# Kernel tuning notes

Hardware: AMD Instinct MI355X
Metric: run time of the kernel (lower is better)

## Reference

```python
import jax, jax.numpy as jnp
import numpy as np

TABLE_SIZE = 256
N_EMBD = 768
B, T = 2, 1024
VOCAB = TABLE_SIZE * TABLE_SIZE


def setup_inputs() -> dict:
    key = jax.random.key(0)
    k1, k2, k3, k4 = jax.random.split(key, 4)
    hidden_states = jax.random.normal(k1, (B, T, N_EMBD), dtype=jnp.float32)
    target_ids = jax.random.randint(k2, (B, T), 0, VOCAB, dtype=jnp.int32).astype(jnp.int64)
    W_row = jax.random.normal(k3, (TABLE_SIZE, N_EMBD), dtype=jnp.float32) * 0.02
    b_row = jnp.zeros((TABLE_SIZE,), dtype=jnp.float32)
    col_weight = jax.random.normal(k4, (TABLE_SIZE, N_EMBD, TABLE_SIZE), dtype=jnp.float32) * 0.02
    col_bias = jnp.zeros((TABLE_SIZE, TABLE_SIZE), dtype=jnp.float32)
    return {
        "hidden_states": hidden_states,
        "target_ids": target_ids,
        "W_row": W_row,
        "b_row": b_row,
        "col_weight": col_weight,
        "col_bias": col_bias,
    }


def reference(hidden_states, target_ids, W_row, b_row, col_weight, col_bias):
    table_size = col_weight.shape[0]
    # row head: (B,T,R)
    row_logits = jnp.einsum("btd,rd->btr", hidden_states, W_row) + b_row
    # codebook.lookup: factor token id over table_size x table_size grid
    row_ids = (target_ids // table_size).reshape(-1)  # (N,)
    col_ids = (target_ids % table_size).reshape(-1)   # (N,)
    hs_flat = hidden_states.reshape(-1, hidden_states.shape[-1])  # (N,d)
    # per-token hard-routed column projection (the gather + baddbmm)
    W_tok = col_weight[row_ids]                       # (N,d,C)
    col_logits = jnp.einsum("nd,ndc->nc", hs_flat, W_tok) + col_bias[row_ids]
    # cross-entropy losses (mean over tokens)
    lp_row = jax.nn.log_softmax(row_logits.reshape(-1, table_size), axis=-1)
    loss_row = -jnp.take_along_axis(lp_row, row_ids[:, None], axis=1).mean()
    lp_col = jax.nn.log_softmax(col_logits, axis=-1)
    loss_col = -jnp.take_along_axis(lp_col, col_ids[:, None], axis=1).mean()
    return loss_row + loss_col
```

## Files before the change

### kernel.cpp

```cpp
#include <hip/hip_runtime.h>
#include <math.h>

#define TABLE 256
#define DIM   768
#define NCH   6
#define DCH   128
#define KTOK  12
#define CAP   64

__device__ __forceinline__ float4 f4zero() { return make_float4(0.f, 0.f, 0.f, 0.f); }

__global__ __launch_bounds__(256) void k_ztrans(
    const float* __restrict__ Wrow,
    float* __restrict__ WrowT,
    int* __restrict__ counts)
{
    const int d = blockIdx.x;
    const int c = threadIdx.x;
    if (d == 0) counts[c] = 0;
    WrowT[(size_t)d * TABLE + c] = Wrow[(size_t)c * DIM + d];
}

__global__ __launch_bounds__(256) void k_bucket(
    const int* __restrict__ tgt, int ntok,
    int* __restrict__ counts, int* __restrict__ bucket)
{
    const int n = blockIdx.x * 256 + threadIdx.x;
    if (n >= ntok) return;
    const int r = tgt[n] >> 8;
    const int pos = atomicAdd(&counts[r], 1);
    if (pos < CAP) bucket[r * CAP + pos] = n;
}

__device__ __forceinline__ void stream_pass(
    const float4* __restrict__ slab4,
    const float*  __restrict__ hs,
    const int* tk,
    int nvalid,
    int dbase,
    float* __restrict__ outp,
    int lane)
{
    int off[KTOK];
    #pragma unroll
    for (int j = 0; j < KTOK; ++j) off[j] = tk[j] * DIM + dbase;

    float4 acc[KTOK];
    #pragma unroll
    for (int j = 0; j < KTOK; ++j) acc[j] = f4zero();

    for (int dq = 0; dq < DCH / 4; ++dq) {
        float4 hv[KTOK];
        #pragma unroll
        for (int j = 0; j < KTOK; ++j)
            hv[j] = reinterpret_cast<const float4*>(hs + off[j])[dq];
        #pragma unroll
        for (int dd = 0; dd < 4; ++dd) {
            const float4 wv = slab4[(size_t)(dq * 4 + dd) * 64 + lane];
            #pragma unroll
            for (int j = 0; j < KTOK; ++j) {
                const float h = (dd == 0) ? hv[j].x : (dd == 1) ? hv[j].y
                              : (dd == 2) ? hv[j].z : hv[j].w;
                acc[j].x = fmaf(h, wv.x, acc[j].x);
                acc[j].y = fmaf(h, wv.y, acc[j].y);
                acc[j].z = fmaf(h, wv.z, acc[j].z);
                acc[j].w = fmaf(h, wv.w, acc[j].w);
            }
        }
    }

    #pragma unroll
    for (int j = 0; j < KTOK; ++j)
        if (j < nvalid)
            reinterpret_cast<float4*>(outp + (size_t)tk[j] * TABLE)[lane] = acc[j];
}

__global__ __launch_bounds__(64) void k_stream(
    const float* __restrict__ hs,
    const float* __restrict__ WrowT,
    const float* __restrict__ CW,
    const int* __restrict__ counts,
    const int* __restrict__ bucket,
    float* __restrict__ row_part,
    float* __restrict__ col_part,
    int ntok)
{
    const int bid  = blockIdx.x;
    const int lane = threadIdx.x;
    const int ncol = 256 * NCH;
    int tk[KTOK];

    if (bid < ncol) {
        const int r     = bid & 255;
        const int chunk = bid >> 8;
        const int cnt = min(counts[r], CAP);
        if (cnt == 0) return;
        const float4* slab4 = reinterpret_cast<const float4*>(
            CW + (size_t)r * DIM * TABLE + (size_t)chunk * DCH * TABLE);
        float* outp = col_part + (size_t)chunk * ntok * TABLE;
        for (int base = 0; base < cnt; base += KTOK) {
            #pragma unroll
            for (int j = 0; j < KTOK; ++j) {
                const int idx = (base + j < cnt) ? (base + j) : base;
                tk[j] = __builtin_amdgcn_readfirstlane(bucket[r * CAP + idx]);
            }
            stream_pass(slab4, hs, tk, min(KTOK, cnt - base),
                        chunk * DCH, outp, lane);
        }
    } else {
        const int b      = bid - ncol;
        const int ntiles = (ntok + KTOK - 1) / KTOK;
        const int tile   = b % ntiles;
        const int chunk  = b / ntiles;
        const int cnt    = min(KTOK, ntok - tile * KTOK);
        #pragma unroll
        for (int j = 0; j < KTOK; ++j) {
            const int idx = (j < cnt) ? j : 0;
            tk[j] = tile * KTOK + idx;
        }
        const float4* slab4 = reinterpret_cast<const float4*>(
            WrowT + (size_t)chunk * DCH * TABLE);
        float* outp = row_part + (size_t)chunk * ntok * TABLE;
        stream_pass(slab4, hs, tk, cnt, chunk * DCH, outp, lane);
    }
}

__device__ __forceinline__ float wave_nll(float4 v, int target, int lane) {
    float m = fmaxf(fmaxf(v.x, v.y), fmaxf(v.z, v.w));
    #pragma unroll
    for (int off = 32; off > 0; off >>= 1) m = fmaxf(m, __shfl_xor(m, off));
    float e = expf(v.x - m) + expf(v.y - m) + expf(v.z - m) + expf(v.w - m);
    float lt = 0.f;
    if (lane == (target >> 2)) {
        const int j = target & 3;
        lt = (j == 0) ? v.x : (j == 1) ? v.y : (j == 2) ? v.z : v.w;
    }
    #pragma unroll
    for (int off = 32; off > 0; off >>= 1) {
        e  += __shfl_xor(e, off);
        lt += __shfl_xor(lt, off);
    }
    return m + logf(e) - lt;
}

__global__ __launch_bounds__(256) void k_nll2(
    const float* __restrict__ row_part,
    const float* __restrict__ col_part,
    const float* __restrict__ brow,
    const float* __restrict__ cbias,
    const int* __restrict__ tgt, int ntok,
    float* __restrict__ per_tok)
{
    const int n = blockIdx.x * 4 + (threadIdx.x >> 6);
    if (n >= ntok) return;
    const int lane = threadIdx.x & 63;
    const int t = tgt[n];
    const int r = t >> 8;

    float4 rl = reinterpret_cast<const float4*>(brow)[lane];
    float4 cl = reinterpret_cast<const float4*>(cbias + (size_t)r * TABLE)[lane];
    #pragma unroll
    for (int ch = 0; ch < NCH; ++ch) {
        const float4 a = reinterpret_cast<const float4*>(
            row_part + ((size_t)ch * ntok + n) * TABLE)[lane];
        const float4 b = reinterpret_cast<const float4*>(
            col_part + ((size_t)ch * ntok + n) * TABLE)[lane];
        rl.x += a.x; rl.y += a.y; rl.z += a.z; rl.w += a.w;
        cl.x += b.x; cl.y += b.y; cl.z += b.z; cl.w += b.w;
    }
    const float lr = wave_nll(rl, r, lane);
    const float lc = wave_nll(cl, t & 255, lane);
    if (lane == 0) per_tok[n] = lr + lc;
}

__global__ __launch_bounds__(256) void k_reduce(
    const float* __restrict__ per_tok, int ntok, float* __restrict__ out)
{
    __shared__ float red[256];
    const int c = threadIdx.x;
    float s = 0.f;
    for (int i = c; i < ntok; i += 256) s += per_tok[i];
    red[c] = s;
    __syncthreads();
    #pragma unroll
    for (int k = 128; k > 0; k >>= 1) {
        if (c < k) red[c] += red[c + k];
        __syncthreads();
    }
    if (c == 0) out[0] = red[0] / (float)ntok;
}

extern "C" void kernel_launch(void* const* d_in, const int* in_sizes, int n_in,
                              void* d_out, int out_size, void* d_ws, size_t ws_size,
                              hipStream_t stream) {
    const float* hs    = (const float*)d_in[0];
    const int*   tgt   = (const int*)d_in[1];
    const float* Wrow  = (const float*)d_in[2];
    const float* brow  = (const float*)d_in[3];
    const float* CW    = (const float*)d_in[4];
    const float* cbias = (const float*)d_in[5];
    float* out = (float*)d_out;

    const int ntok = in_sizes[1];

    char* ws = (char*)d_ws;
    int*   counts   = (int*)(ws);
    int*   bucket   = (int*)(ws + 1024);
    float* WrowT    = (float*)(ws + 1024 + 256 * CAP * 4);
    char*  p0       = (char*)WrowT + (size_t)DIM * TABLE * 4;
    float* row_part = (float*)p0;
    float* col_part = row_part + (size_t)NCH * ntok * TABLE;
    float* per_tok  = col_part + (size_t)NCH * ntok * TABLE;

    const int ntiles = (ntok + KTOK - 1) / KTOK;
    const int nblk   = 256 * NCH + ntiles * NCH;

    k_ztrans <<<DIM, 256, 0, stream>>>(Wrow, WrowT, counts);
    k_bucket <<<(ntok + 255) / 256, 256, 0, stream>>>(tgt, ntok, counts, bucket);
    k_stream <<<nblk, 64, 0, stream>>>(hs, WrowT, CW, counts, bucket,
                                       row_part, col_part, ntok);
    k_nll2   <<<(ntok + 3) / 4, 256, 0, stream>>>(row_part, col_part, brow, cbias,
                                                  tgt, ntok, per_tok);
    k_reduce <<<1, 256, 0, stream>>>(per_tok, ntok, out);
}
```

Before: 82.07 us.

## Split column dimension across two waves per block-chunk in stream kernel

Each k_stream block now covers half of the 256 output columns (float2 per lane instead of float4), and twice as many blocks are launched. This halves per-thread accumulator registers and doubles parallelism, which should improve occupancy and latency hiding. The cost is that each block re-reads the hidden-state vectors for its tokens, so hs traffic doubles, and per-lane weight loads become narrower. An unroll-2 hint is also added to the d loop.

```diff
diff --git a/kernel.cpp b/kernel.cpp
--- a/kernel.cpp
+++ b/kernel.cpp
@@ -8,7 +8,7 @@
 #define KTOK  12
 #define CAP   64
 
-__device__ __forceinline__ float4 f4zero() { return make_float4(0.f, 0.f, 0.f, 0.f); }
+__device__ __forceinline__ float2 f2zero() { return make_float2(0.f, 0.f); }
 
 __global__ __launch_bounds__(256) void k_ztrans(
     const float* __restrict__ Wrow,
@@ -33,11 +33,12 @@
 }
 
 __device__ __forceinline__ void stream_pass(
-    const float4* __restrict__ slab4,
-    const float*  __restrict__ hs,
+    const float* __restrict__ slab,
+    const float* __restrict__ hs,
     const int* tk,
     int nvalid,
     int dbase,
+    int cbase,
     float* __restrict__ outp,
     int lane)
 {
@@ -45,10 +46,13 @@
     #pragma unroll
     for (int j = 0; j < KTOK; ++j) off[j] = tk[j] * DIM + dbase;
 
-    float4 acc[KTOK];
-    #pragma unroll
-    for (int j = 0; j < KTOK; ++j) acc[j] = f4zero();
-
+    float2 acc[KTOK];
+    #pragma unroll
+    for (int j = 0; j < KTOK; ++j) acc[j] = f2zero();
+
+    const float* sl = slab + cbase + 2 * lane;
+
+    #pragma unroll 2
     for (int dq = 0; dq < DCH / 4; ++dq) {
         float4 hv[KTOK];
         #pragma unroll
@@ -56,15 +60,14 @@
             hv[j] = reinterpret_cast<const float4*>(hs + off[j])[dq];
         #pragma unroll
         for (int dd = 0; dd < 4; ++dd) {
-            const float4 wv = slab4[(size_t)(dq * 4 + dd) * 64 + lane];
+            const float2 wv = *reinterpret_cast<const float2*>(
+                sl + (size_t)(dq * 4 + dd) * TABLE);
             #pragma unroll
             for (int j = 0; j < KTOK; ++j) {
                 const float h = (dd == 0) ? hv[j].x : (dd == 1) ? hv[j].y
                               : (dd == 2) ? hv[j].z : hv[j].w;
                 acc[j].x = fmaf(h, wv.x, acc[j].x);
                 acc[j].y = fmaf(h, wv.y, acc[j].y);
-                acc[j].z = fmaf(h, wv.z, acc[j].z);
-                acc[j].w = fmaf(h, wv.w, acc[j].w);
             }
         }
     }
@@ -72,7 +75,8 @@
     #pragma unroll
     for (int j = 0; j < KTOK; ++j)
         if (j < nvalid)
-            reinterpret_cast<float4*>(outp + (size_t)tk[j] * TABLE)[lane] = acc[j];
+            *reinterpret_cast<float2*>(outp + (size_t)tk[j] * TABLE + cbase + 2 * lane)
+                = acc[j];
 }
 
 __global__ __launch_bounds__(64) void k_stream(
@@ -87,16 +91,17 @@
 {
     const int bid  = blockIdx.x;
     const int lane = threadIdx.x;
-    const int ncol = 256 * NCH;
+    const int ncol = 256 * NCH * 2;
     int tk[KTOK];
 
     if (bid < ncol) {
         const int r     = bid & 255;
-        const int chunk = bid >> 8;
+        const int rest  = bid >> 8;
+        const int chunk = rest >> 1;
+        const int cbase = (rest & 1) * 128;
         const int cnt = min(counts[r], CAP);
         if (cnt == 0) return;
-        const float4* slab4 = reinterpret_cast<const float4*>(
-            CW + (size_t)r * DIM * TABLE + (size_t)chunk * DCH * TABLE);
+        const float* slab = CW + (size_t)r * DIM * TABLE + (size_t)chunk * DCH * TABLE;
         float* outp = col_part + (size_t)chunk * ntok * TABLE;
         for (int base = 0; base < cnt; base += KTOK) {
             #pragma unroll
@@ -104,24 +109,25 @@
                 const int idx = (base + j < cnt) ? (base + j) : base;
                 tk[j] = __builtin_amdgcn_readfirstlane(bucket[r * CAP + idx]);
             }
-            stream_pass(slab4, hs, tk, min(KTOK, cnt - base),
-                        chunk * DCH, outp, lane);
+            stream_pass(slab, hs, tk, min(KTOK, cnt - base),
+                        chunk * DCH, cbase, outp, lane);
         }
     } else {
         const int b      = bid - ncol;
         const int ntiles = (ntok + KTOK - 1) / KTOK;
         const int tile   = b % ntiles;
-        const int chunk  = b / ntiles;
+        const int rest   = b / ntiles;
+        const int chunk  = rest >> 1;
+        const int cbase  = (rest & 1) * 128;
         const int cnt    = min(KTOK, ntok - tile * KTOK);
         #pragma unroll
         for (int j = 0; j < KTOK; ++j) {
             const int idx = (j < cnt) ? j : 0;
             tk[j] = tile * KTOK + idx;
         }
-        const float4* slab4 = reinterpret_cast<const float4*>(
-            WrowT + (size_t)chunk * DCH * TABLE);
+        const float* slab = WrowT + (size_t)chunk * DCH * TABLE;
         float* outp = row_part + (size_t)chunk * ntok * TABLE;
-        stream_pass(slab4, hs, tk, cnt, chunk * DCH, outp, lane);
+        stream_pass(slab, hs, tk, cnt, chunk * DCH, cbase, outp, lane);
     }
 }
 
@@ -213,7 +219,7 @@
     float* per_tok  = col_part + (size_t)NCH * ntok * TABLE;
 
     const int ntiles = (ntok + KTOK - 1) / KTOK;
-    const int nblk   = 256 * NCH + ntiles * NCH;
+    const int nblk   = 256 * NCH * 2 + ntiles * NCH * 2;
 
     k_ztrans <<<DIM, 256, 0, stream>>>(Wrow, WrowT, counts);
     k_bucket <<<(ntok + 255) / 256, 256, 0, stream>>>(tgt, ntok, counts, bucket);
```

After: 76.27 us. -7.1%, faster.

## Stage weight slab through LDS with async global_load_lds ring buffer

Applied to the files above, without the earlier changes.

Hidden-state chunks for the token tile are staged into shared memory once per pass. Weight slab rows are prefetched into a 16-row LDS ring using global-to-LDS async loads, with manual vmcnt waits so loads overlap the FMA compute. The aim is to hide global memory latency in the per-row streaming kernel. It adds LDS usage, hand-tuned waitcnt sequencing that is fragile, and extra LDS read traffic.

```diff
diff --git a/kernel.cpp b/kernel.cpp
--- a/kernel.cpp
+++ b/kernel.cpp
@@ -7,8 +7,7 @@
 #define DCH   128
 #define KTOK  12
 #define CAP   64
-
-__device__ __forceinline__ float4 f4zero() { return make_float4(0.f, 0.f, 0.f, 0.f); }
+#define WIN   16
 
 __global__ __launch_bounds__(256) void k_ztrans(
     const float* __restrict__ Wrow,
@@ -32,42 +31,85 @@
     if (pos < CAP) bucket[r * CAP + pos] = n;
 }
 
+__device__ __forceinline__ void async_row(const float* g, float4* l, int lane) {
+    __builtin_amdgcn_global_load_lds(
+        (const __attribute__((address_space(1))) void*)(g + 4 * lane),
+        (__attribute__((address_space(3))) void*)l, 16, 0, 0);
+}
+
 __device__ __forceinline__ void stream_pass(
-    const float4* __restrict__ slab4,
-    const float*  __restrict__ hs,
+    const float* __restrict__ slab,
+    const float* __restrict__ hs,
     const int* tk,
     int nvalid,
     int dbase,
+    float4 (*slab_lds)[64],
+    float* hs_lds,
     float* __restrict__ outp,
     int lane)
 {
-    int off[KTOK];
-    #pragma unroll
-    for (int j = 0; j < KTOK; ++j) off[j] = tk[j] * DIM + dbase;
+    const int half = lane >> 5;
+    const int q    = lane & 31;
+    #pragma unroll
+    for (int i = 0; i < KTOK / 2; ++i) {
+        const int tt = (half == 0) ? tk[2 * i] : tk[2 * i + 1];
+        const float4 v = *reinterpret_cast<const float4*>(
+            hs + (size_t)tt * DIM + dbase + 4 * q);
+        *reinterpret_cast<float4*>(hs_lds + (2 * i + half) * DCH + 4 * q) = v;
+    }
+    asm volatile("s_waitcnt vmcnt(0) lgkmcnt(0)" ::: "memory");
+
+    #pragma unroll
+    for (int r = 0; r < WIN; ++r)
+        async_row(slab + (size_t)r * TABLE, &slab_lds[r][0], lane);
 
     float4 acc[KTOK];
     #pragma unroll
-    for (int j = 0; j < KTOK; ++j) acc[j] = f4zero();
-
-    for (int dq = 0; dq < DCH / 4; ++dq) {
+    for (int j = 0; j < KTOK; ++j) acc[j] = make_float4(0.f, 0.f, 0.f, 0.f);
+
+    auto compute_group = [&](int g) {
         float4 hv[KTOK];
         #pragma unroll
         for (int j = 0; j < KTOK; ++j)
-            hv[j] = reinterpret_cast<const float4*>(hs + off[j])[dq];
+            hv[j] = *reinterpret_cast<const float4*>(hs_lds + j * DCH + 4 * g);
         #pragma unroll
-        for (int dd = 0; dd < 4; ++dd) {
-            const float4 wv = slab4[(size_t)(dq * 4 + dd) * 64 + lane];
+        for (int k = 0; k < 4; ++k) {
+            const float4 wv = slab_lds[(4 * g + k) & (WIN - 1)][lane];
             #pragma unroll
             for (int j = 0; j < KTOK; ++j) {
-                const float h = (dd == 0) ? hv[j].x : (dd == 1) ? hv[j].y
-                              : (dd == 2) ? hv[j].z : hv[j].w;
+                const float h = (k == 0) ? hv[j].x : (k == 1) ? hv[j].y
+                              : (k == 2) ? hv[j].z : hv[j].w;
                 acc[j].x = fmaf(h, wv.x, acc[j].x);
                 acc[j].y = fmaf(h, wv.y, acc[j].y);
                 acc[j].z = fmaf(h, wv.z, acc[j].z);
                 acc[j].w = fmaf(h, wv.w, acc[j].w);
             }
         }
-    }
+    };
+
+    for (int g = 0; g < 29; ++g) {
+        asm volatile("s_waitcnt vmcnt(12)" ::: "memory");
+        __builtin_amdgcn_sched_barrier(0);
+        compute_group(g);
+        asm volatile("s_waitcnt lgkmcnt(0)" ::: "memory");
+        if (g < 28) {
+            const int ir = WIN + 4 * g;
+            #pragma unroll
+            for (int k = 0; k < 4; ++k)
+                async_row(slab + (size_t)(ir + k) * TABLE,
+                          &slab_lds[(ir + k) & (WIN - 1)][0], lane);
+        }
+    }
+    asm volatile("s_waitcnt vmcnt(8)" ::: "memory");
+    __builtin_amdgcn_sched_barrier(0);
+    compute_group(29);
+    asm volatile("s_waitcnt vmcnt(4)" ::: "memory");
+    __builtin_amdgcn_sched_barrier(0);
+    compute_group(30);
+    asm volatile("s_waitcnt vmcnt(0)" ::: "memory");
+    __builtin_amdgcn_sched_barrier(0);
+    compute_group(31);
+    asm volatile("s_waitcnt lgkmcnt(0)" ::: "memory");
 
     #pragma unroll
     for (int j = 0; j < KTOK; ++j)
@@ -85,6 +127,9 @@
     float* __restrict__ col_part,
     int ntok)
 {
+    __shared__ float4 slab_lds[WIN][64];
+    __shared__ float  hs_lds[KTOK * DCH];
+
     const int bid  = blockIdx.x;
     const int lane = threadIdx.x;
     const int ncol = 256 * NCH;
@@ -95,8 +140,7 @@
         const int chunk = bid >> 8;
         const int cnt = min(counts[r], CAP);
         if (cnt == 0) return;
-        const float4* slab4 = reinterpret_cast<const float4*>(
-            CW + (size_t)r * DIM * TABLE + (size_t)chunk * DCH * TABLE);
+        const float* slab = CW + (size_t)r * DIM * TABLE + (size_t)chunk * DCH * TABLE;
         float* outp = col_part + (size_t)chunk * ntok * TABLE;
         for (int base = 0; base < cnt; base += KTOK) {
             #pragma unroll
@@ -104,12 +148,13 @@
                 const int idx = (base + j < cnt) ? (base + j) : base;
                 tk[j] = __builtin_amdgcn_readfirstlane(bucket[r * CAP + idx]);
             }
-            stream_pass(slab4, hs, tk, min(KTOK, cnt - base),
-                        chunk * DCH, outp, lane);
+            stream_pass(slab, hs, tk, min(KTOK, cnt - base),
+                        chunk * DCH, slab_lds, hs_lds, outp, lane);
         }
     } else {
         const int b      = bid - ncol;
         const int ntiles = (ntok + KTOK - 1) / KTOK;
+        if (b >= ntiles * NCH) return;
         const int tile   = b % ntiles;
         const int chunk  = b / ntiles;
         const int cnt    = min(KTOK, ntok - tile * KTOK);
@@ -118,10 +163,9 @@
             const int idx = (j < cnt) ? j : 0;
             tk[j] = tile * KTOK + idx;
         }
-        const float4* slab4 = reinterpret_cast<const float4*>(
-            WrowT + (size_t)chunk * DCH * TABLE);
+        const float* slab = WrowT + (size_t)chunk * DCH * TABLE;
         float* outp = row_part + (size_t)chunk * ntok * TABLE;
-        stream_pass(slab4, hs, tk, cnt, chunk * DCH, outp, lane);
+        stream_pass(slab, hs, tk, cnt, chunk * DCH, slab_lds, hs_lds, outp, lane);
     }
 }
 
```

New measurement: 72.28 us. -11.9%, faster.
